# Kernel optimization log

Hardware: AMD Instinct MI355X
Metric: run time of the kernel (lower is better)

Reference implementation:

```python
import jax, jax.numpy as jnp
import numpy as np

def setup_inputs() -> dict:
    key = jax.random.key(0)
    x = jax.random.normal(key, (4096, 3, 64, 64), dtype=jnp.float32)
    return {"x": x}

def reference(x):
    # x: [N, C=3, H, W]; attention runs over the N dim with feature dim H*W
    N, C, H, W = x.shape
    out = x.reshape(N, C, H * W)          # [N, 3, HW]
    q, k, v = out[:, 0], out[:, 1], out[:, 2]  # each [N, HW]
    dp = (q @ k.T) * 0.5                  # [N, N]
    attn = jax.nn.softmax(dp, axis=-1)
    # dropout omitted (eval-mode / deterministic reference)
    return attn @ v                       # [N, HW]
```

## Files before the change

kernel.cpp:

```cpp
#include <hip/hip_runtime.h>
#include <hip/hip_bf16.h>
#include <cstdint>

#define N 4096
#define ROWSTRIDE 12288

typedef __attribute__((ext_vector_type(8))) _Float16 half8;
typedef __attribute__((ext_vector_type(4))) _Float16 half4v;
typedef __attribute__((ext_vector_type(4))) float floatx4;

__global__ __launch_bounds__(256) void pack_qk(const float* __restrict__ x,
                                               _Float16* __restrict__ qh,
                                               _Float16* __restrict__ kh) {
    const size_t tid = (size_t)blockIdx.x * 256 + threadIdx.x;
    const int i  = (int)(tid >> 10);
    const int c4 = (int)(tid & 1023);
    const float4* xr = (const float4*)(x + (size_t)i * ROWSTRIDE);
    float4 q = xr[c4];
    float4 k = xr[1024 + c4];
    half4v qo = {(_Float16)(q.x * 0.5f), (_Float16)(q.y * 0.5f),
                 (_Float16)(q.z * 0.5f), (_Float16)(q.w * 0.5f)};
    half4v ko = {(_Float16)k.x, (_Float16)k.y, (_Float16)k.z, (_Float16)k.w};
    *(half4v*)(qh + tid * 4) = qo;
    *(half4v*)(kh + tid * 4) = ko;
}

__global__ __launch_bounds__(256) void transpose_v(const float* __restrict__ x,
                                                   _Float16* __restrict__ vt) {
    __shared__ float tile[32][33];
    const int j0 = blockIdx.x * 32;
    const int d0 = blockIdx.y * 32;
    const int t  = threadIdx.x;
    const int r  = t >> 3;
    const int c4 = t & 7;
    const float4 val = *(const float4*)(x + (size_t)(j0 + r) * ROWSTRIDE + 8192 + d0 + c4 * 4);
    tile[r][c4 * 4 + 0] = val.x;
    tile[r][c4 * 4 + 1] = val.y;
    tile[r][c4 * 4 + 2] = val.z;
    tile[r][c4 * 4 + 3] = val.w;
    __syncthreads();
    half4v o = {(_Float16)tile[c4 * 4 + 0][r], (_Float16)tile[c4 * 4 + 1][r],
                (_Float16)tile[c4 * 4 + 2][r], (_Float16)tile[c4 * 4 + 3][r]};
    *(half4v*)(vt + (size_t)(d0 + r) * N + j0 + c4 * 4) = o;
}

#define GL2LDS(g, l)                                                                     \
    __builtin_amdgcn_global_load_lds((const __attribute__((address_space(1))) void*)(g), \
                                     (__attribute__((address_space(3))) void*)(l), 16, 0, 0)

__global__ __launch_bounds__(256) void gemm_nt(const _Float16* __restrict__ A,
                                               const _Float16* __restrict__ Bt,
                                               float* __restrict__ C) {
    __shared__ _Float16 As[2 * 128 * 32];
    __shared__ _Float16 Bs[2 * 128 * 32];
    const int t    = threadIdx.x;
    const int wave = t >> 6;
    const int lane = t & 63;
    const int wr   = wave >> 1, wc = wave & 1;
    const int rowBase = blockIdx.y * 128;
    const int colBase = blockIdx.x * 128;

    floatx4 acc[4][4] = {};

    const int ldRow = t >> 2;
    const int ldCol = (t & 3) * 8;
    const _Float16* ga0 = A  + (size_t)(rowBase + ldRow) * N + ldCol;
    const _Float16* gb0 = Bt + (size_t)(colBase + ldRow) * N + ldCol;
    _Float16* lA = &As[wave * 512];
    _Float16* lB = &Bs[wave * 512];

    const int fr = lane & 15;
    const int fk = (lane >> 4) * 8;

    for (int kt = 0; kt < 64; ++kt) {
        const int k0 = kt * 64;
        __syncthreads();
        GL2LDS(ga0 + k0, lA);
        GL2LDS(ga0 + k0 + (size_t)64 * N, lA + 2048);
        GL2LDS(gb0 + k0, lB);
        GL2LDS(gb0 + k0 + (size_t)64 * N, lB + 2048);
        GL2LDS(ga0 + k0 + 32, lA + 4096);
        GL2LDS(ga0 + k0 + 32 + (size_t)64 * N, lA + 6144);
        GL2LDS(gb0 + k0 + 32, lB + 4096);
        GL2LDS(gb0 + k0 + 32 + (size_t)64 * N, lB + 6144);
        __syncthreads();

#pragma unroll
        for (int ks = 0; ks < 2; ++ks) {
            half8 af[4], bf[4];
#pragma unroll
            for (int mt = 0; mt < 4; ++mt)
                af[mt] = *(half8*)&As[ks * 4096 + (wr * 64 + mt * 16 + fr) * 32 + fk];
#pragma unroll
            for (int nt = 0; nt < 4; ++nt)
                bf[nt] = *(half8*)&Bs[ks * 4096 + (wc * 64 + nt * 16 + fr) * 32 + fk];
#pragma unroll
            for (int mt = 0; mt < 4; ++mt)
#pragma unroll
                for (int nt = 0; nt < 4; ++nt)
                    acc[mt][nt] = __builtin_amdgcn_mfma_f32_16x16x32_f16(af[mt], bf[nt],
                                                                         acc[mt][nt], 0, 0, 0);
        }
    }

    const int quad = lane >> 4;
#pragma unroll
    for (int mt = 0; mt < 4; ++mt) {
#pragma unroll
        for (int nt = 0; nt < 4; ++nt) {
#pragma unroll
            for (int r = 0; r < 4; ++r) {
                const int row = rowBase + wr * 64 + mt * 16 + quad * 4 + r;
                const int col = colBase + wc * 64 + nt * 16 + fr;
                C[(size_t)row * N + col] = acc[mt][nt][r];
            }
        }
    }
}

__global__ __launch_bounds__(256) void softmax_rows(const float* __restrict__ S,
                                                    _Float16* __restrict__ P) {
    const int row = blockIdx.x;
    const int t   = threadIdx.x;
    const float4* Sr = (const float4*)(S + (size_t)row * N);

    float4 v[4];
    float lmax = -3.0e38f;
#pragma unroll
    for (int r = 0; r < 4; ++r) {
        v[r] = Sr[t + 256 * r];
        lmax = fmaxf(lmax, fmaxf(fmaxf(v[r].x, v[r].y), fmaxf(v[r].z, v[r].w)));
    }
#pragma unroll
    for (int off = 32; off; off >>= 1) lmax = fmaxf(lmax, __shfl_xor(lmax, off, 64));
    __shared__ float redm[4], reds[4];
    const int wave = t >> 6, lane = t & 63;
    if (lane == 0) redm[wave] = lmax;
    __syncthreads();
    const float m = fmaxf(fmaxf(redm[0], redm[1]), fmaxf(redm[2], redm[3]));

    float lsum = 0.f;
#pragma unroll
    for (int r = 0; r < 4; ++r) {
        v[r].x = __expf(v[r].x - m);
        v[r].y = __expf(v[r].y - m);
        v[r].z = __expf(v[r].z - m);
        v[r].w = __expf(v[r].w - m);
        lsum += (v[r].x + v[r].y) + (v[r].z + v[r].w);
    }
#pragma unroll
    for (int off = 32; off; off >>= 1) lsum += __shfl_xor(lsum, off, 64);
    if (lane == 0) reds[wave] = lsum;
    __syncthreads();
    const float inv = 1.0f / (((reds[0] + reds[1]) + (reds[2] + reds[3])));

#pragma unroll
    for (int r = 0; r < 4; ++r) {
        half4v o = {(_Float16)(v[r].x * inv), (_Float16)(v[r].y * inv),
                    (_Float16)(v[r].z * inv), (_Float16)(v[r].w * inv)};
        *(half4v*)(P + (size_t)row * N + (t + 256 * r) * 4) = o;
    }
}

extern "C" void kernel_launch(void* const* d_in, const int* in_sizes, int n_in,
                              void* d_out, int out_size, void* d_ws, size_t ws_size,
                              hipStream_t stream) {
    const float* x = (const float*)d_in[0];
    float* out     = (float*)d_out;
    char* ws       = (char*)d_ws;

    _Float16* qh = (_Float16*)(ws);
    _Float16* kh = (_Float16*)(ws + (32ull << 20));
    _Float16* vt = (_Float16*)(ws + (64ull << 20));
    float*    S  = (float*)   (ws + (96ull << 20));
    _Float16* P  = qh;

    pack_qk    <<<16384, 256, 0, stream>>>(x, qh, kh);
    transpose_v<<<dim3(128, 128), 256, 0, stream>>>(x, vt);
    gemm_nt    <<<dim3(32, 32), 256, 0, stream>>>(qh, kh, S);
    softmax_rows<<<4096, 256, 0, stream>>>(S, P);
    gemm_nt    <<<dim3(32, 32), 256, 0, stream>>>(P, vt, out);
}
```

Measured before the change: 646.3 us.

## Double-buffer LDS tiles in gemm_nt to overlap global loads with MFMA

The GEMM kernel now keeps two LDS buffers for the A and B tiles. It issues the global-to-LDS loads for the next K-tile before computing on the current one, which removes one barrier per iteration and lets the loads run behind the MFMA work. The cost is that LDS per block doubles to 64KB, which lowers the number of resident blocks per CU. The overlap only happens if the compiler does not insert a conservative vmcnt wait before the LDS reads.

```diff
diff --git a/kernel.cpp b/kernel.cpp
--- a/kernel.cpp
+++ b/kernel.cpp
@@ -51,8 +51,8 @@
 __global__ __launch_bounds__(256) void gemm_nt(const _Float16* __restrict__ A,
                                                const _Float16* __restrict__ Bt,
                                                float* __restrict__ C) {
-    __shared__ _Float16 As[2 * 128 * 32];
-    __shared__ _Float16 Bs[2 * 128 * 32];
+    __shared__ _Float16 As[2][2 * 128 * 32];
+    __shared__ _Float16 Bs[2][2 * 128 * 32];
     const int t    = threadIdx.x;
     const int wave = t >> 6;
     const int lane = t & 63;
@@ -66,34 +66,39 @@
     const int ldCol = (t & 3) * 8;
     const _Float16* ga0 = A  + (size_t)(rowBase + ldRow) * N + ldCol;
     const _Float16* gb0 = Bt + (size_t)(colBase + ldRow) * N + ldCol;
-    _Float16* lA = &As[wave * 512];
-    _Float16* lB = &Bs[wave * 512];
+    const int wbase = wave * 512;
 
     const int fr = lane & 15;
     const int fk = (lane >> 4) * 8;
 
+    auto stage = [&](int k0, _Float16* dA, _Float16* dB) {
+        GL2LDS(ga0 + k0, dA);
+        GL2LDS(ga0 + k0 + (size_t)64 * N, dA + 2048);
+        GL2LDS(gb0 + k0, dB);
+        GL2LDS(gb0 + k0 + (size_t)64 * N, dB + 2048);
+        GL2LDS(ga0 + k0 + 32, dA + 4096);
+        GL2LDS(ga0 + k0 + 32 + (size_t)64 * N, dA + 6144);
+        GL2LDS(gb0 + k0 + 32, dB + 4096);
+        GL2LDS(gb0 + k0 + 32 + (size_t)64 * N, dB + 6144);
+    };
+
+    stage(0, &As[0][wbase], &Bs[0][wbase]);
+
     for (int kt = 0; kt < 64; ++kt) {
-        const int k0 = kt * 64;
+        const int p = kt & 1;
         __syncthreads();
-        GL2LDS(ga0 + k0, lA);
-        GL2LDS(ga0 + k0 + (size_t)64 * N, lA + 2048);
-        GL2LDS(gb0 + k0, lB);
-        GL2LDS(gb0 + k0 + (size_t)64 * N, lB + 2048);
-        GL2LDS(ga0 + k0 + 32, lA + 4096);
-        GL2LDS(ga0 + k0 + 32 + (size_t)64 * N, lA + 6144);
-        GL2LDS(gb0 + k0 + 32, lB + 4096);
-        GL2LDS(gb0 + k0 + 32 + (size_t)64 * N, lB + 6144);
-        __syncthreads();
+        if (kt < 63)
+            stage((kt + 1) * 64, &As[p ^ 1][wbase], &Bs[p ^ 1][wbase]);
 
 #pragma unroll
         for (int ks = 0; ks < 2; ++ks) {
             half8 af[4], bf[4];
 #pragma unroll
             for (int mt = 0; mt < 4; ++mt)
-                af[mt] = *(half8*)&As[ks * 4096 + (wr * 64 + mt * 16 + fr) * 32 + fk];
+                af[mt] = *(half8*)&As[p][ks * 4096 + (wr * 64 + mt * 16 + fr) * 32 + fk];
 #pragma unroll
             for (int nt = 0; nt < 4; ++nt)
-                bf[nt] = *(half8*)&Bs[ks * 4096 + (wc * 64 + nt * 16 + fr) * 32 + fk];
+                bf[nt] = *(half8*)&Bs[p][ks * 4096 + (wc * 64 + nt * 16 + fr) * 32 + fk];
 #pragma unroll
             for (int mt = 0; mt < 4; ++mt)
 #pragma unroll
```

After: 715.2 us. 1.11x slower.
